# Kernel tuning notes

Measured on AMD Instinct MI355X. Metric: run time of the kernel, lower is better.

Reference implementation:

```python
import jax, jax.numpy as jnp
import numpy as np
from jax import lax

B = 16
T_MEL = 16
FEAT = 80
BITS = 9
N_CLASSES = 2 ** BITS  # 512
RNN = 512
SCALES = (5, 5, 11)
PAD = 2
TOTAL_SCALE = 275      # prod(SCALES)
INDENT = PAD * TOTAL_SCALE  # 550
T = (T_MEL - 2 * PAD) * TOTAL_SCALE  # 3300
D_IN = FEAT + N_CLASSES  # 592 = GRU input size


def setup_inputs() -> dict:
    key = jax.random.key(0)
    ks = jax.random.split(key, 10)
    s = 0.05
    inp = {
        "x": jax.random.randint(ks[0], (B, T), 0, N_CLASSES),
        "mels": jax.random.normal(ks[1], (B, FEAT, T_MEL), jnp.float32),
    }
    # upsample conv kernels: Conv2d(1,1,(1,2s+1)) with weight filled 1/(2s+1)
    for i, sc in enumerate(SCALES):
        k = 2 * sc + 1
        inp[f"up_k{i}"] = jnp.full((1, 1, 1, k), 1.0 / k, jnp.float32)
    # GRU (torch layout: [3H, in], gates ordered r,z,n)
    inp["w_ih"] = jax.random.normal(ks[2], (3 * RNN, D_IN), jnp.float32) * s
    inp["w_hh"] = jax.random.normal(ks[3], (3 * RNN, RNN), jnp.float32) * s
    inp["b_ih"] = jax.random.normal(ks[4], (3 * RNN,), jnp.float32) * s
    inp["b_hh"] = jax.random.normal(ks[5], (3 * RNN,), jnp.float32) * s
    # fc1: Linear(rnn_dims, n_classes); fc2: Linear(n_classes, n_classes)
    inp["fc1_w"] = jax.random.normal(ks[6], (N_CLASSES, RNN), jnp.float32) * s
    inp["fc1_b"] = jax.random.normal(ks[7], (N_CLASSES,), jnp.float32) * s
    inp["fc2_w"] = jax.random.normal(ks[8], (N_CLASSES, N_CLASSES), jnp.float32) * s
    inp["fc2_b"] = jax.random.normal(ks[9], (N_CLASSES,), jnp.float32) * s
    return inp


def _upsample_mels(mels, kernels):
    # m-path of UpsampleNetwork: Stretch2d(scale,1) + averaging Conv2d per scale
    m = mels[:, None]  # [B,1,FEAT,T_MEL]
    for sc, k in zip(SCALES, kernels):
        m = jnp.repeat(m, sc, axis=-1)  # Stretch2d along time
        m = lax.conv_general_dilated(
            m, k, window_strides=(1, 1), padding=[(0, 0), (sc, sc)],
            dimension_numbers=("NCHW", "OIHW", "NCHW"))
    m = m[:, 0, :, INDENT:-INDENT]  # [B, FEAT, T]
    return jnp.transpose(m, (0, 2, 1))  # [B, T, FEAT]


def _gru(xin, w_ih, w_hh, b_ih, b_hh):
    # precompute input projection for all timesteps: [B,T,3H]
    x_proj = jnp.einsum("btd,gd->btg", xin, w_ih) + b_ih

    def step(h, xp):  # xp: [B,3H]
        hp = h @ w_hh.T + b_hh
        xr, xz, xn = jnp.split(xp, 3, axis=-1)
        hr, hz, hn = jnp.split(hp, 3, axis=-1)
        r = jax.nn.sigmoid(xr + hr)
        z = jax.nn.sigmoid(xz + hz)
        n = jnp.tanh(xn + r * hn)
        h_new = (1.0 - z) * n + z * h
        return h_new, h_new

    h0 = jnp.zeros((xin.shape[0], RNN), xin.dtype)
    _, hs = lax.scan(step, h0, jnp.transpose(x_proj, (1, 0, 2)))  # [T,B,H]
    return jnp.transpose(hs, (1, 0, 2))  # [B,T,H]


def reference(x, mels, up_k0, up_k1, up_k2,
              w_ih, w_hh, b_ih, b_hh, fc1_w, fc1_b, fc2_w, fc2_b):
    # vectorized replacement for the per-element scatter loop: one-hot of x
    netinput = jax.nn.one_hot(x, N_CLASSES, dtype=jnp.float32)  # [B,T,C]
    mels_up = _upsample_mels(mels, (up_k0, up_k1, up_k2))       # [B,T,FEAT]
    xin = jnp.concatenate([netinput, mels_up], axis=2)          # [B,T,C+FEAT]
    h = _gru(xin, w_ih, w_hh, b_ih, b_hh)                       # [B,T,RNN]
    h = jax.nn.relu(jnp.einsum("bth,fh->btf", h, fc1_w) + fc1_b)
    out = jnp.einsum("btf,cf->btc", h, fc2_w) + fc2_b           # [B,T,C]
    return out
```

## Files before the change

### kernel.cpp

```cpp
#include <hip/hip_runtime.h>
#include <stdint.h>

typedef unsigned short ushort_t;
typedef unsigned long long u64;
typedef __attribute__((ext_vector_type(8))) short short8;
typedef __attribute__((ext_vector_type(4))) float f32x4;

#define T_SEQ 3300
#define SENT 0x7FC00001u
#define SENTPAIR 0x7FC000017FC00001ull

__device__ __forceinline__ ushort_t f2b(float f) {
  uint32_t u = __float_as_uint(f);
  u = (u + 0x7fffu + ((u >> 16) & 1u)) >> 16;
  return (ushort_t)u;
}
__device__ __forceinline__ float b2f(ushort_t b) {
  return __uint_as_float(((uint32_t)b) << 16);
}

__global__ void prep_kernel(const float* __restrict__ w_ih,
                            const float* __restrict__ fc1w,
                            const float* __restrict__ fc2w,
                            ushort_t* __restrict__ w_ihT,
                            ushort_t* __restrict__ fc1wb,
                            ushort_t* __restrict__ fc2wb,
                            uint32_t* __restrict__ h_ring) {
  int i = blockIdx.x * 256 + threadIdx.x;
  if (i < 512 * 1536) {
    int d = i / 1536, g = i - d * 1536;
    w_ihT[i] = f2b(w_ih[g * 592 + d]);
  }
  int j = i - 512 * 1536;
  if (j >= 0 && j < 262144) fc1wb[j] = f2b(fc1w[j]);
  int k = j - 262144;
  if (k >= 0 && k < 262144) fc2wb[k] = f2b(fc2w[k]);
  int c = k - 262144;
  if (c >= 0 && c < 131072) {
    __hip_atomic_store(&h_ring[c], SENT, __ATOMIC_RELAXED, __HIP_MEMORY_SCOPE_AGENT);
  }
}

__global__ void upsample_kernel(const float* __restrict__ mels,
                                const float* __restrict__ k0,
                                const float* __restrict__ k1,
                                const float* __restrict__ k2,
                                float* __restrict__ mels_up) {
  __shared__ float s0[16];
  __shared__ float s1[80];
  __shared__ float s2[400];
  int bf = blockIdx.x;
  int b = bf / 80, f = bf - b * 80;
  int tid = threadIdx.x;
  float c0 = k0[0], c1 = k1[0], c2 = k2[0];
  if (tid < 16) s0[tid] = mels[(b * 80 + f) * 16 + tid];
  __syncthreads();
  if (tid < 80) {
    float a = 0.f;
    #pragma unroll
    for (int d = -5; d <= 5; ++d) {
      int w = tid + d;
      if (w >= 0 && w < 80) a += s0[w / 5];
    }
    s1[tid] = a * c0;
  }
  __syncthreads();
  for (int w = tid; w < 400; w += 128) {
    float a = 0.f;
    #pragma unroll
    for (int d = -5; d <= 5; ++d) {
      int u = w + d;
      if (u >= 0 && u < 400) a += s1[u / 5];
    }
    s2[w] = a * c1;
  }
  __syncthreads();
  for (int t = tid; t < T_SEQ; t += 128) {
    int wb = 550 + t;
    float a = 0.f;
    #pragma unroll
    for (int d = -11; d <= 11; ++d) a += s2[(wb + d) / 11];
    mels_up[(b * 80 + f) * T_SEQ + t] = a * c2;
  }
}

__device__ __forceinline__ float red32(float x) {
  x += __uint_as_float((uint32_t)__builtin_amdgcn_update_dpp(0, (int)__float_as_uint(x), 0x111, 0xf, 0xf, true));
  x += __uint_as_float((uint32_t)__builtin_amdgcn_update_dpp(0, (int)__float_as_uint(x), 0x112, 0xf, 0xf, true));
  x += __uint_as_float((uint32_t)__builtin_amdgcn_update_dpp(0, (int)__float_as_uint(x), 0x114, 0xf, 0xf, true));
  x += __uint_as_float((uint32_t)__builtin_amdgcn_update_dpp(0, (int)__float_as_uint(x), 0x118, 0xf, 0xf, true));
  x += __shfl_xor(x, 16, 64);
  return x;
}

__global__ __launch_bounds__(512) void gru_kernel(
    const int* __restrict__ x,
    const float* __restrict__ mels_up,
    const float* __restrict__ w_ih,
    const float* __restrict__ w_hh,
    const float* __restrict__ b_ih,
    const float* __restrict__ b_hh,
    const ushort_t* __restrict__ w_ihT,
    uint32_t* __restrict__ h_ring,
    ushort_t* __restrict__ h_seq)
{
  int blk = blockIdx.x;
  int xcd = blk & 7, slot = blk >> 3;
  int b = (xcd << 1) | (slot >> 4);
  int j = slot & 15;
  int tid = threadIdx.x;
  int cc = tid & 31, rr = tid >> 5;

  __shared__ __align__(16) float v[640];
  __shared__ float embs[96];

  if (tid < 48) v[592 + tid] = 0.f;

  float w[6][20];
  float wmel[2][3];
  float bsum[4], bihn[2], bhhn[2];
  #pragma unroll
  for (int q = 0; q < 6; ++q) {
    int gate = q >> 1, kk = q & 1;
    int g = gate * 512 + j * 32 + rr * 2 + kk;
    #pragma unroll
    for (int cl = 0; cl < 20; ++cl) {
      int col = cc * 20 + cl;
      float wv = 0.f;
      if (col < 512) wv = w_hh[g * 512 + col];
      else if (col < 592 && gate < 2) wv = w_ih[g * 592 + col];
      w[q][cl] = wv;
    }
  }
  #pragma unroll
  for (int kk = 0; kk < 2; ++kk) {
    int g = 1024 + j * 32 + rr * 2 + kk;
    #pragma unroll
    for (int ii = 0; ii < 3; ++ii) {
      int fidx = cc * 3 + ii;
      wmel[kk][ii] = (fidx < 80) ? w_ih[g * 592 + 512 + fidx] : 0.f;
    }
    bihn[kk] = b_ih[g];
    bhhn[kk] = b_hh[g];
  }
  #pragma unroll
  for (int q = 0; q < 4; ++q) {
    int gate = q >> 1, kk = q & 1;
    int g = gate * 512 + j * 32 + rr * 2 + kk;
    bsum[q] = b_ih[g] + b_hh[g];
  }

  for (int t = 0; t < T_SEQ; ++t) {
    float melv = 0.f;
    if (tid < 80) melv = mels_up[(b * 80 + tid) * T_SEQ + t];
    float embv = 0.f;
    if (tid < 96) {
      int xv = x[b * T_SEQ + t];
      int gate = tid >> 5, kl = tid & 31;
      embv = b2f(w_ihT[xv * 1536 + gate * 512 + j * 32 + kl]);
    }
    u64 q0 = 0, q1 = 0;
    if (t > 0 && tid < 128) {
      int rslot = (t - 1) & 15;
      const u64* src = (const u64*)&h_ring[((rslot * 16 + b) * 512) + tid * 4];
      for (;;) {
        q0 = __hip_atomic_load(src,     __ATOMIC_RELAXED, __HIP_MEMORY_SCOPE_AGENT);
        q1 = __hip_atomic_load(src + 1, __ATOMIC_RELAXED, __HIP_MEMORY_SCOPE_AGENT);
        if (((uint32_t)q0) != SENT && ((uint32_t)(q0 >> 32)) != SENT &&
            ((uint32_t)q1) != SENT && ((uint32_t)(q1 >> 32)) != SENT) break;
      }
    }
    if (tid < 128) {
      ((u64*)v)[tid * 2]     = q0;
      ((u64*)v)[tid * 2 + 1] = q1;
    }
    if (tid < 80) v[512 + tid] = melv;
    if (tid < 96) embs[tid] = embv;
    __syncthreads();

    float hv20[20];
    #pragma unroll
    for (int s = 0; s < 5; ++s) {
      f32x4 t4 = *(const f32x4*)&v[cc * 20 + s * 4];
      hv20[s * 4 + 0] = t4[0]; hv20[s * 4 + 1] = t4[1];
      hv20[s * 4 + 2] = t4[2]; hv20[s * 4 + 3] = t4[3];
    }
    float a0 = 0.f, a1 = 0.f, a2 = 0.f, a3 = 0.f, a4 = 0.f, a5 = 0.f;
    #pragma unroll
    for (int cl = 0; cl < 20; ++cl) {
      float hvv = hv20[cl];
      a0 += hvv * w[0][cl]; a1 += hvv * w[1][cl];
      a2 += hvv * w[2][cl]; a3 += hvv * w[3][cl];
      a4 += hvv * w[4][cl]; a5 += hvv * w[5][cl];
    }
    float am0 = 0.f, am1 = 0.f;
    #pragma unroll
    for (int ii = 0; ii < 3; ++ii) {
      float mv = v[512 + cc * 3 + ii];
      am0 += mv * wmel[0][ii]; am1 += mv * wmel[1][ii];
    }
    float r0 = red32(a0), r1 = red32(a1), r2 = red32(a2);
    float r3 = red32(a3), r4 = red32(a4), r5 = red32(a5);
    float rm0 = red32(am0), rm1 = red32(am1);

    if (cc == 15) {
      float hn2[2];
      #pragma unroll
      for (int kk = 0; kk < 2; ++kk) {
        float sr  = kk ? r1 : r0;
        float sz  = kk ? r3 : r2;
        float sn  = kk ? r5 : r4;
        float smn = kk ? rm1 : rm0;
        int k = rr * 2 + kk;
        float ar = embs[k] + sr + bsum[0 + kk];
        float az = embs[32 + k] + sz + bsum[2 + kk];
        float rg = 1.f / (1.f + __expf(-ar));
        float zg = 1.f / (1.f + __expf(-az));
        float xn = embs[64 + k] + smn + bihn[kk];
        float hn = sn + bhhn[kk];
        float na = xn + rg * hn;
        float e2 = __expf(2.f * na);
        float ng = 1.f - 2.f / (e2 + 1.f);
        float hp = v[j * 32 + k];
        hn2[kk] = (1.f - zg) * ng + zg * hp;
      }
      int wslot = t & 15;
      u64 pk = ((u64)__float_as_uint(hn2[1]) << 32) | (u64)__float_as_uint(hn2[0]);
      u64* dst = (u64*)&h_ring[((wslot * 16 + b) * 512) + j * 32 + rr * 2];
      __hip_atomic_store(dst, pk, __ATOMIC_RELAXED, __HIP_MEMORY_SCOPE_AGENT);
      int aslot = (t + 8) & 15;
      u64* adst = (u64*)&h_ring[((aslot * 16 + b) * 512) + j * 32 + rr * 2];
      __hip_atomic_store(adst, SENTPAIR, __ATOMIC_RELAXED, __HIP_MEMORY_SCOPE_AGENT);
      uint32_t hb = (uint32_t)f2b(hn2[0]) | ((uint32_t)f2b(hn2[1]) << 16);
      *(uint32_t*)&h_seq[(size_t)(b * T_SEQ + t) * 512 + j * 32 + rr * 2] = hb;
    }
    __syncthreads();
  }
}

__global__ __launch_bounds__(512) void head_kernel(
    const ushort_t* __restrict__ h_seq,
    const ushort_t* __restrict__ fc1w,
    const ushort_t* __restrict__ fc2w,
    const float* __restrict__ fc1b,
    const float* __restrict__ fc2b,
    float* __restrict__ out) {
  __shared__ __align__(16) ushort_t h1[64 * 512];
  int blk = blockIdx.x;
  int tid = threadIdx.x;
  int w = tid >> 6, l = tid & 63;
  int lm = l & 15, lq = l >> 4;
  int mt = w & 3;
  int nb = (w >> 2) * 256;
  int m0 = blk * 64;

  f32x4 acc[16];
  #pragma unroll
  for (int i = 0; i < 16; ++i) acc[i] = (f32x4){0.f, 0.f, 0.f, 0.f};
  const ushort_t* arow = h_seq + (size_t)(m0 + mt * 16 + lm) * 512;
  for (int kt = 0; kt < 16; ++kt) {
    short8 a = *(const short8*)(arow + kt * 32 + lq * 8);
    #pragma unroll
    for (int nt = 0; nt < 16; ++nt) {
      short8 bb = *(const short8*)(fc1w + (size_t)(nb + nt * 16 + lm) * 512 + kt * 32 + lq * 8);
      acc[nt] = __builtin_amdgcn_mfma_f32_16x16x32_bf16(a, bb, acc[nt], 0, 0, 0);
    }
  }
  #pragma unroll
  for (int nt = 0; nt < 16; ++nt) {
    int n = nb + nt * 16 + lm;
    float bias = fc1b[n];
    #pragma unroll
    for (int r = 0; r < 4; ++r) {
      int m = mt * 16 + lq * 4 + r;
      float vv = acc[nt][r] + bias;
      vv = fmaxf(vv, 0.f);
      h1[m * 512 + n] = f2b(vv);
    }
  }
  __syncthreads();
  f32x4 acc2[16];
  #pragma unroll
  for (int i = 0; i < 16; ++i) acc2[i] = (f32x4){0.f, 0.f, 0.f, 0.f};
  for (int kt = 0; kt < 16; ++kt) {
    short8 a = *(const short8*)&h1[(mt * 16 + lm) * 512 + kt * 32 + lq * 8];
    #pragma unroll
    for (int nt = 0; nt < 16; ++nt) {
      short8 bb = *(const short8*)(fc2w + (size_t)(nb + nt * 16 + lm) * 512 + kt * 32 + lq * 8);
      acc2[nt] = __builtin_amdgcn_mfma_f32_16x16x32_bf16(a, bb, acc2[nt], 0, 0, 0);
    }
  }
  #pragma unroll
  for (int nt = 0; nt < 16; ++nt) {
    int n = nb + nt * 16 + lm;
    float bias = fc2b[n];
    #pragma unroll
    for (int r = 0; r < 4; ++r) {
      int m = mt * 16 + lq * 4 + r;
      out[(size_t)(m0 + m) * 512 + n] = acc2[nt][r] + bias;
    }
  }
}

extern "C" void kernel_launch(void* const* d_in, const int* in_sizes, int n_in,
                              void* d_out, int out_size, void* d_ws, size_t ws_size,
                              hipStream_t stream) {
  (void)in_sizes; (void)n_in; (void)out_size; (void)ws_size;
  const int*   x    = (const int*)d_in[0];
  const float* mels = (const float*)d_in[1];
  const float* k0   = (const float*)d_in[2];
  const float* k1   = (const float*)d_in[3];
  const float* k2   = (const float*)d_in[4];
  const float* w_ih = (const float*)d_in[5];
  const float* w_hh = (const float*)d_in[6];
  const float* b_ih = (const float*)d_in[7];
  const float* b_hh = (const float*)d_in[8];
  const float* fc1w = (const float*)d_in[9];
  const float* fc1b = (const float*)d_in[10];
  const float* fc2w = (const float*)d_in[11];
  const float* fc2b = (const float*)d_in[12];

  char* ws = (char*)d_ws;
  float*    mels_up = (float*)(ws + 0);
  ushort_t* h_seq   = (ushort_t*)(ws + 16896000);
  ushort_t* w_ihT   = (ushort_t*)(ws + 70963200);
  ushort_t* fc1wb   = (ushort_t*)(ws + 72536064);
  ushort_t* fc2wb   = (ushort_t*)(ws + 73060352);
  uint32_t* h_ring  = (uint32_t*)(ws + 73584640);

  prep_kernel<<<5632, 256, 0, stream>>>(w_ih, fc1w, fc2w, w_ihT, fc1wb, fc2wb, h_ring);
  upsample_kernel<<<1280, 128, 0, stream>>>(mels, k0, k1, k2, mels_up);
  gru_kernel<<<256, 512, 0, stream>>>(x, mels_up, w_ih, w_hh, b_ih, b_hh, w_ihT,
                                      h_ring, h_seq);
  head_kernel<<<825, 512, 0, stream>>>(h_seq, fc1wb, fc2wb, fc1b, fc2b, (float*)d_out);
}
```

Baseline: 6.790 ms.

## Batch GRU recurrence across all sequences with split-bf16 MFMA in 32 blocks

Replaces the per-batch scalar FMA GRU (256 blocks, one batch each) with 32 blocks that each own 16 hidden units for all 16 batches. The hidden-state matvec becomes a 16x16 MFMA tile using a three-term hi/lo bf16 split to keep near-fp32 accuracy. The mel input is transposed for coalesced per-step loads, and the h_ring now stores packed hi/lo bf16 pairs. This cuts the number of cross-block communicating blocks and the per-step reduction cost, at the price of three MFMAs per tile and staging split weights in the tail of the output buffer before the head overwrites it.

```diff
diff --git a/kernel.cpp b/kernel.cpp
--- a/kernel.cpp
+++ b/kernel.cpp
@@ -8,7 +8,7 @@
 
 #define T_SEQ 3300
 #define SENT 0x7FC00001u
-#define SENTPAIR 0x7FC000017FC00001ull
+#define OUT_BYTES 108134400ull
 
 __device__ __forceinline__ ushort_t f2b(float f) {
   uint32_t u = __float_as_uint(f);
@@ -20,18 +20,38 @@
 }
 
 __global__ void prep_kernel(const float* __restrict__ w_ih,
+                            const float* __restrict__ w_hh,
                             const float* __restrict__ fc1w,
                             const float* __restrict__ fc2w,
                             ushort_t* __restrict__ w_ihT,
+                            ushort_t* __restrict__ whh_hi,
+                            ushort_t* __restrict__ whh_lo,
+                            ushort_t* __restrict__ wmel_hi,
+                            ushort_t* __restrict__ wmel_lo,
                             ushort_t* __restrict__ fc1wb,
                             ushort_t* __restrict__ fc2wb,
                             uint32_t* __restrict__ h_ring) {
   int i = blockIdx.x * 256 + threadIdx.x;
-  if (i < 512 * 1536) {
+  if (i < 786432) {
     int d = i / 1536, g = i - d * 1536;
     w_ihT[i] = f2b(w_ih[g * 592 + d]);
   }
-  int j = i - 512 * 1536;
+  int a = i - 786432;
+  if (a >= 0 && a < 786432) {
+    float v = w_hh[a];
+    ushort_t h = f2b(v);
+    whh_hi[a] = h;
+    whh_lo[a] = f2b(v - b2f(h));
+  }
+  int m = a - 786432;
+  if (m >= 0 && m < 147456) {
+    int g = m / 96, f = m - g * 96;
+    float v = (f < 80) ? w_ih[g * 592 + 512 + f] : 0.f;
+    ushort_t h = f2b(v);
+    wmel_hi[m] = h;
+    wmel_lo[m] = f2b(v - b2f(h));
+  }
+  int j = m - 147456;
   if (j >= 0 && j < 262144) fc1wb[j] = f2b(fc1w[j]);
   int k = j - 262144;
   if (k >= 0 && k < 262144) fc2wb[k] = f2b(fc2w[k]);
@@ -45,7 +65,7 @@
                                 const float* __restrict__ k0,
                                 const float* __restrict__ k1,
                                 const float* __restrict__ k2,
-                                float* __restrict__ mels_up) {
+                                float* __restrict__ mels_upT) {
   __shared__ float s0[16];
   __shared__ float s1[80];
   __shared__ float s2[400];
@@ -80,159 +100,199 @@
     float a = 0.f;
     #pragma unroll
     for (int d = -11; d <= 11; ++d) a += s2[(wb + d) / 11];
-    mels_up[(b * 80 + f) * T_SEQ + t] = a * c2;
-  }
-}
-
-__device__ __forceinline__ float red32(float x) {
-  x += __uint_as_float((uint32_t)__builtin_amdgcn_update_dpp(0, (int)__float_as_uint(x), 0x111, 0xf, 0xf, true));
-  x += __uint_as_float((uint32_t)__builtin_amdgcn_update_dpp(0, (int)__float_as_uint(x), 0x112, 0xf, 0xf, true));
-  x += __uint_as_float((uint32_t)__builtin_amdgcn_update_dpp(0, (int)__float_as_uint(x), 0x114, 0xf, 0xf, true));
-  x += __uint_as_float((uint32_t)__builtin_amdgcn_update_dpp(0, (int)__float_as_uint(x), 0x118, 0xf, 0xf, true));
-  x += __shfl_xor(x, 16, 64);
-  return x;
+    mels_upT[t * 1280 + b * 80 + f] = a * c2;
+  }
 }
 
 __global__ __launch_bounds__(512) void gru_kernel(
     const int* __restrict__ x,
-    const float* __restrict__ mels_up,
-    const float* __restrict__ w_ih,
-    const float* __restrict__ w_hh,
+    const float* __restrict__ mels_upT,
     const float* __restrict__ b_ih,
     const float* __restrict__ b_hh,
     const ushort_t* __restrict__ w_ihT,
+    const ushort_t* __restrict__ whh_hi,
+    const ushort_t* __restrict__ whh_lo,
+    const ushort_t* __restrict__ wmel_hi,
+    const ushort_t* __restrict__ wmel_lo,
     uint32_t* __restrict__ h_ring,
     ushort_t* __restrict__ h_seq)
 {
   int blk = blockIdx.x;
-  int xcd = blk & 7, slot = blk >> 3;
-  int b = (xcd << 1) | (slot >> 4);
-  int j = slot & 15;
   int tid = threadIdx.x;
-  int cc = tid & 31, rr = tid >> 5;
-
-  __shared__ __align__(16) float v[640];
-  __shared__ float embs[96];
-
-  if (tid < 48) v[592 + tid] = 0.f;
-
-  float w[6][20];
-  float wmel[2][3];
-  float bsum[4], bihn[2], bhhn[2];
-  #pragma unroll
-  for (int q = 0; q < 6; ++q) {
-    int gate = q >> 1, kk = q & 1;
-    int g = gate * 512 + j * 32 + rr * 2 + kk;
-    #pragma unroll
-    for (int cl = 0; cl < 20; ++cl) {
-      int col = cc * 20 + cl;
-      float wv = 0.f;
-      if (col < 512) wv = w_hh[g * 512 + col];
-      else if (col < 592 && gate < 2) wv = w_ih[g * 592 + col];
-      w[q][cl] = wv;
-    }
-  }
-  #pragma unroll
-  for (int kk = 0; kk < 2; ++kk) {
-    int g = 1024 + j * 32 + rr * 2 + kk;
-    #pragma unroll
-    for (int ii = 0; ii < 3; ++ii) {
-      int fidx = cc * 3 + ii;
-      wmel[kk][ii] = (fidx < 80) ? w_ih[g * 592 + 512 + fidx] : 0.f;
-    }
-    bihn[kk] = b_ih[g];
-    bhhn[kk] = b_hh[g];
-  }
-  #pragma unroll
-  for (int q = 0; q < 4; ++q) {
-    int gate = q >> 1, kk = q & 1;
-    int g = gate * 512 + j * 32 + rr * 2 + kk;
-    bsum[q] = b_ih[g] + b_hh[g];
+  int lane = tid & 63, wv = tid >> 6;
+  int lm = lane & 15, lq = lane >> 4;
+  int pb = tid >> 5, pc = tid & 31;
+  int gb = tid >> 4, gd = tid & 15;
+
+  __shared__ __align__(16) ushort_t Hhi[16][520];
+  __shared__ __align__(16) ushort_t Hlo[16][520];
+  __shared__ __align__(16) ushort_t Mhi[16][104];
+  __shared__ __align__(16) ushort_t Mlo[16][104];
+  __shared__ float Cred[9][16][16];
+  __shared__ int xvbuf[16];
+
+  for (int idx = tid; idx < 16 * 24; idx += 512) {
+    int b = idx / 24, f = 80 + (idx - b * 24);
+    Mhi[b][f] = 0; Mlo[b][f] = 0;
+  }
+
+  int nt = wv >> 1, kh = wv & 1;
+  short8 wbh[8], wbl[8];
+  if (wv < 6) {
+    int row = nt * 512 + blk * 16 + lm;
+    #pragma unroll
+    for (int k8 = 0; k8 < 8; ++k8) {
+      int kt = kh * 8 + k8;
+      wbh[k8] = *(const short8*)(whh_hi + (size_t)row * 512 + kt * 32 + lq * 8);
+      wbl[k8] = *(const short8*)(whh_lo + (size_t)row * 512 + kt * 32 + lq * 8);
+    }
+  }
+  short8 wmh[2][3], wml[2][3];
+  if (wv >= 6) {
+    #pragma unroll
+    for (int u = 0; u < 2; ++u) {
+      int nt2 = (wv == 6) ? u : 2;
+      int row = nt2 * 512 + blk * 16 + lm;
+      #pragma unroll
+      for (int kt = 0; kt < 3; ++kt) {
+        wmh[u][kt] = *(const short8*)(wmel_hi + (size_t)row * 96 + kt * 32 + lq * 8);
+        wml[u][kt] = *(const short8*)(wmel_lo + (size_t)row * 96 + kt * 32 + lq * 8);
+      }
+    }
+  }
+  float h_prev = 0.f, bsr = 0.f, bsz = 0.f, bihn_ = 0.f, bhhn_ = 0.f;
+  if (tid < 256) {
+    int gr = blk * 16 + gd;
+    bsr = b_ih[gr] + b_hh[gr];
+    bsz = b_ih[512 + gr] + b_hh[512 + gr];
+    bihn_ = b_ih[1024 + gr];
+    bhhn_ = b_hh[1024 + gr];
   }
 
   for (int t = 0; t < T_SEQ; ++t) {
-    float melv = 0.f;
-    if (tid < 80) melv = mels_up[(b * 80 + tid) * T_SEQ + t];
-    float embv = 0.f;
-    if (tid < 96) {
-      int xv = x[b * T_SEQ + t];
-      int gate = tid >> 5, kl = tid & 31;
-      embv = b2f(w_ihT[xv * 1536 + gate * 512 + j * 32 + kl]);
-    }
-    u64 q0 = 0, q1 = 0;
-    if (t > 0 && tid < 128) {
-      int rslot = (t - 1) & 15;
-      const u64* src = (const u64*)&h_ring[((rslot * 16 + b) * 512) + tid * 4];
-      for (;;) {
-        q0 = __hip_atomic_load(src,     __ATOMIC_RELAXED, __HIP_MEMORY_SCOPE_AGENT);
-        q1 = __hip_atomic_load(src + 1, __ATOMIC_RELAXED, __HIP_MEMORY_SCOPE_AGENT);
-        if (((uint32_t)q0) != SENT && ((uint32_t)(q0 >> 32)) != SENT &&
-            ((uint32_t)q1) != SENT && ((uint32_t)(q1 >> 32)) != SENT) break;
-      }
-    }
-    if (tid < 128) {
-      ((u64*)v)[tid * 2]     = q0;
-      ((u64*)v)[tid * 2 + 1] = q1;
-    }
-    if (tid < 80) v[512 + tid] = melv;
-    if (tid < 96) embs[tid] = embv;
+    int rslot = (t - 1) & 15, wslot = t & 15, aslot = (t + 8) & 15;
+    f32x4 ma = {0.f, 0.f, 0.f, 0.f}, mb = {0.f, 0.f, 0.f, 0.f};
+    if (tid < 160) {
+      const float* mp = mels_upT + (size_t)t * 1280 + tid * 8;
+      ma = *(const f32x4*)mp;
+      mb = *(const f32x4*)(mp + 4);
+    }
+    if (tid < 16) xvbuf[tid] = x[tid * T_SEQ + t];
+
+    u64 q[8];
+    #pragma unroll
+    for (int jj = 0; jj < 8; ++jj) q[jj] = 0;
+    if (t > 0) {
+      const u64* src = (const u64*)&h_ring[((rslot * 16 + pb) << 9) + pc * 16];
+      for (int spin = 0; spin < 4096; ++spin) {
+        bool ok = true;
+        #pragma unroll
+        for (int jj = 0; jj < 8; ++jj) {
+          q[jj] = __hip_atomic_load(src + jj, __ATOMIC_RELAXED, __HIP_MEMORY_SCOPE_AGENT);
+          ok = ok && (((uint32_t)q[jj]) != SENT) && (((uint32_t)(q[jj] >> 32)) != SENT);
+        }
+        if (ok) break;
+      }
+    }
+    {
+      uint32_t* hrow = (uint32_t*)&Hhi[pb][0];
+      uint32_t* lrow = (uint32_t*)&Hlo[pb][0];
+      #pragma unroll
+      for (int jj = 0; jj < 8; ++jj) {
+        uint32_t w0 = (uint32_t)q[jj], w1 = (uint32_t)(q[jj] >> 32);
+        hrow[pc * 8 + jj] = (w0 & 0xFFFFu) | (w1 << 16);
+        lrow[pc * 8 + jj] = (w0 >> 16) | (w1 & 0xFFFF0000u);
+      }
+    }
+    if (tid < 160) {
+      short8 hv, lv;
+      #pragma unroll
+      for (int e = 0; e < 4; ++e) {
+        ushort_t h0 = f2b(ma[e]);
+        hv[e] = (short)h0; lv[e] = (short)f2b(ma[e] - b2f(h0));
+        ushort_t h1 = f2b(mb[e]);
+        hv[4 + e] = (short)h1; lv[4 + e] = (short)f2b(mb[e] - b2f(h1));
+      }
+      int mbb = tid / 10, mf = (tid - mbb * 10) * 8;
+      *(short8*)&Mhi[mbb][mf] = hv;
+      *(short8*)&Mlo[mbb][mf] = lv;
+    }
     __syncthreads();
 
-    float hv20[20];
-    #pragma unroll
-    for (int s = 0; s < 5; ++s) {
-      f32x4 t4 = *(const f32x4*)&v[cc * 20 + s * 4];
-      hv20[s * 4 + 0] = t4[0]; hv20[s * 4 + 1] = t4[1];
-      hv20[s * 4 + 2] = t4[2]; hv20[s * 4 + 3] = t4[3];
-    }
-    float a0 = 0.f, a1 = 0.f, a2 = 0.f, a3 = 0.f, a4 = 0.f, a5 = 0.f;
-    #pragma unroll
-    for (int cl = 0; cl < 20; ++cl) {
-      float hvv = hv20[cl];
-      a0 += hvv * w[0][cl]; a1 += hvv * w[1][cl];
-      a2 += hvv * w[2][cl]; a3 += hvv * w[3][cl];
-      a4 += hvv * w[4][cl]; a5 += hvv * w[5][cl];
-    }
-    float am0 = 0.f, am1 = 0.f;
-    #pragma unroll
-    for (int ii = 0; ii < 3; ++ii) {
-      float mv = v[512 + cc * 3 + ii];
-      am0 += mv * wmel[0][ii]; am1 += mv * wmel[1][ii];
-    }
-    float r0 = red32(a0), r1 = red32(a1), r2 = red32(a2);
-    float r3 = red32(a3), r4 = red32(a4), r5 = red32(a5);
-    float rm0 = red32(am0), rm1 = red32(am1);
-
-    if (cc == 15) {
-      float hn2[2];
-      #pragma unroll
-      for (int kk = 0; kk < 2; ++kk) {
-        float sr  = kk ? r1 : r0;
-        float sz  = kk ? r3 : r2;
-        float sn  = kk ? r5 : r4;
-        float smn = kk ? rm1 : rm0;
-        int k = rr * 2 + kk;
-        float ar = embs[k] + sr + bsum[0 + kk];
-        float az = embs[32 + k] + sz + bsum[2 + kk];
-        float rg = 1.f / (1.f + __expf(-ar));
-        float zg = 1.f / (1.f + __expf(-az));
-        float xn = embs[64 + k] + smn + bihn[kk];
-        float hn = sn + bhhn[kk];
-        float na = xn + rg * hn;
-        float e2 = __expf(2.f * na);
-        float ng = 1.f - 2.f / (e2 + 1.f);
-        float hp = v[j * 32 + k];
-        hn2[kk] = (1.f - zg) * ng + zg * hp;
-      }
-      int wslot = t & 15;
-      u64 pk = ((u64)__float_as_uint(hn2[1]) << 32) | (u64)__float_as_uint(hn2[0]);
-      u64* dst = (u64*)&h_ring[((wslot * 16 + b) * 512) + j * 32 + rr * 2];
-      __hip_atomic_store(dst, pk, __ATOMIC_RELAXED, __HIP_MEMORY_SCOPE_AGENT);
-      int aslot = (t + 8) & 15;
-      u64* adst = (u64*)&h_ring[((aslot * 16 + b) * 512) + j * 32 + rr * 2];
-      __hip_atomic_store(adst, SENTPAIR, __ATOMIC_RELAXED, __HIP_MEMORY_SCOPE_AGENT);
-      uint32_t hb = (uint32_t)f2b(hn2[0]) | ((uint32_t)f2b(hn2[1]) << 16);
-      *(uint32_t*)&h_seq[(size_t)(b * T_SEQ + t) * 512 + j * 32 + rr * 2] = hb;
+    float embr = 0.f, embz = 0.f, embn = 0.f;
+    if (tid < 256) {
+      int xv = xvbuf[gb];
+      const ushort_t* er = w_ihT + (size_t)xv * 1536 + blk * 16 + gd;
+      embr = b2f(er[0]);
+      embz = b2f(er[512]);
+      embn = b2f(er[1024]);
+    }
+    if (wv < 6) {
+      short8 ah[8], al[8];
+      #pragma unroll
+      for (int k8 = 0; k8 < 8; ++k8) {
+        int kk = (kh * 8 + k8) * 32 + lq * 8;
+        ah[k8] = *(const short8*)&Hhi[lm][kk];
+        al[k8] = *(const short8*)&Hlo[lm][kk];
+      }
+      f32x4 ce = {0.f, 0.f, 0.f, 0.f}, co = {0.f, 0.f, 0.f, 0.f};
+      #pragma unroll
+      for (int k8 = 0; k8 < 8; ++k8) {
+        ce = __builtin_amdgcn_mfma_f32_16x16x32_bf16(ah[k8], wbh[k8], ce, 0, 0, 0);
+        co = __builtin_amdgcn_mfma_f32_16x16x32_bf16(al[k8], wbh[k8], co, 0, 0, 0);
+        ce = __builtin_amdgcn_mfma_f32_16x16x32_bf16(ah[k8], wbl[k8], ce, 0, 0, 0);
+      }
+      #pragma unroll
+      for (int r = 0; r < 4; ++r) Cred[wv][lq * 4 + r][lm] = ce[r] + co[r];
+    } else {
+      short8 amh[3], aml[3];
+      #pragma unroll
+      for (int kt = 0; kt < 3; ++kt) {
+        amh[kt] = *(const short8*)&Mhi[lm][kt * 32 + lq * 8];
+        aml[kt] = *(const short8*)&Mlo[lm][kt * 32 + lq * 8];
+      }
+      #pragma unroll
+      for (int u = 0; u < 2; ++u) {
+        if (!(wv == 7 && u == 1)) {
+          f32x4 cm = {0.f, 0.f, 0.f, 0.f};
+          #pragma unroll
+          for (int kt = 0; kt < 3; ++kt) {
+            cm = __builtin_amdgcn_mfma_f32_16x16x32_bf16(amh[kt], wmh[u][kt], cm, 0, 0, 0);
+            cm = __builtin_amdgcn_mfma_f32_16x16x32_bf16(aml[kt], wmh[u][kt], cm, 0, 0, 0);
+            cm = __builtin_amdgcn_mfma_f32_16x16x32_bf16(amh[kt], wml[u][kt], cm, 0, 0, 0);
+          }
+          int cslot = (wv == 6) ? (6 + u) : 8;
+          #pragma unroll
+          for (int r = 0; r < 4; ++r) Cred[cslot][lq * 4 + r][lm] = cm[r];
+        }
+      }
+    }
+    __syncthreads();
+
+    if (tid < 256) {
+      float hr = Cred[0][gb][gd] + Cred[1][gb][gd];
+      float hz = Cred[2][gb][gd] + Cred[3][gb][gd];
+      float hn = Cred[4][gb][gd] + Cred[5][gb][gd];
+      float mr = Cred[6][gb][gd], mz = Cred[7][gb][gd], mn = Cred[8][gb][gd];
+      float ar = embr + mr + hr + bsr;
+      float az = embz + mz + hz + bsz;
+      float rg = 1.f / (1.f + __expf(-ar));
+      float zg = 1.f / (1.f + __expf(-az));
+      float xn = embn + mn + bihn_;
+      float hns = hn + bhhn_;
+      float na = xn + rg * hns;
+      float e2 = __expf(2.f * na);
+      float ng = 1.f - 2.f / (e2 + 1.f);
+      float h = (1.f - zg) * ng + zg * h_prev;
+      h_prev = h;
+      ushort_t hib = f2b(h);
+      ushort_t lob = f2b(h - b2f(hib));
+      uint32_t pk = (uint32_t)hib | ((uint32_t)lob << 16);
+      __hip_atomic_store(&h_ring[((wslot * 16 + gb) << 9) + blk * 16 + gd], pk,
+                         __ATOMIC_RELAXED, __HIP_MEMORY_SCOPE_AGENT);
+      __hip_atomic_store(&h_ring[((aslot * 16 + gb) << 9) + blk * 16 + gd], SENT,
+                         __ATOMIC_RELAXED, __HIP_MEMORY_SCOPE_AGENT);
+      h_seq[(size_t)(gb * T_SEQ + t) * 512 + blk * 16 + gd] = hib;
     }
     __syncthreads();
   }
@@ -321,16 +381,25 @@
   const float* fc2b = (const float*)d_in[12];
 
   char* ws = (char*)d_ws;
-  float*    mels_up = (float*)(ws + 0);
-  ushort_t* h_seq   = (ushort_t*)(ws + 16896000);
-  ushort_t* w_ihT   = (ushort_t*)(ws + 70963200);
-  ushort_t* fc1wb   = (ushort_t*)(ws + 72536064);
-  ushort_t* fc2wb   = (ushort_t*)(ws + 73060352);
-  uint32_t* h_ring  = (uint32_t*)(ws + 73584640);
-
-  prep_kernel<<<5632, 256, 0, stream>>>(w_ih, fc1w, fc2w, w_ihT, fc1wb, fc2wb, h_ring);
-  upsample_kernel<<<1280, 128, 0, stream>>>(mels, k0, k1, k2, mels_up);
-  gru_kernel<<<256, 512, 0, stream>>>(x, mels_up, w_ih, w_hh, b_ih, b_hh, w_ihT,
-                                      h_ring, h_seq);
+  float*    mels_upT = (float*)(ws + 0);
+  ushort_t* h_seq    = (ushort_t*)(ws + 16896000);
+  ushort_t* w_ihT    = (ushort_t*)(ws + 70963200);
+  ushort_t* fc1wb    = (ushort_t*)(ws + 72536064);
+  ushort_t* fc2wb    = (ushort_t*)(ws + 73060352);
+  uint32_t* h_ring   = (uint32_t*)(ws + 73584640);
+
+  char* ob = (char*)d_out;
+  ushort_t* whh_hi  = (ushort_t*)(ob + OUT_BYTES - 3735552);
+  ushort_t* whh_lo  = (ushort_t*)(ob + OUT_BYTES - 2162688);
+  ushort_t* wmel_hi = (ushort_t*)(ob + OUT_BYTES -  589824);
+  ushort_t* wmel_lo = (ushort_t*)(ob + OUT_BYTES -  294912);
+
+  prep_kernel<<<9280, 256, 0, stream>>>(w_ih, w_hh, fc1w, fc2w, w_ihT,
+                                        whh_hi, whh_lo, wmel_hi, wmel_lo,
+                                        fc1wb, fc2wb, h_ring);
+  upsample_kernel<<<1280, 128, 0, stream>>>(mels, k0, k1, k2, mels_upT);
+  gru_kernel<<<32, 512, 0, stream>>>(x, mels_upT, b_ih, b_hh, w_ihT,
+                                     whh_hi, whh_lo, wmel_hi, wmel_lo,
+                                     h_ring, h_seq);
   head_kernel<<<825, 512, 0, stream>>>(h_seq, fc1wb, fc2wb, fc1b, fc2b, (float*)d_out);
 }
```

Result: slower. 11.10 ms (+63.4%).
